# Optimization experiments

Measured on AMD Instinct MI355X. Metric: run time of the kernel, lower is better.

## Reference

```python
import jax, jax.numpy as jnp
import numpy as np

B, L, S, D, H, DH = 32, 96, 96, 512, 8, 64  # d_ff = S*S = 9216


def setup_inputs() -> dict:
    key = jax.random.key(0)
    ks = jax.random.split(key, 13)
    sc = 0.02
    inp = {
        "queries": jax.random.normal(ks[0], (B, L, D), jnp.float32),
        "keys": jax.random.normal(ks[1], (B, S, D), jnp.float32),
        "values": jax.random.normal(ks[2], (B, S, D), jnp.float32),
        "attn_mask": jnp.zeros((B, L, S), dtype=bool),
        # projections stored as (in, out); torch Linear is x @ W.T + b
        "Wq": jax.random.normal(ks[3], (D, H * DH), jnp.float32) * sc,
        "bq": jnp.zeros((H * DH,), jnp.float32),
        "Wk": jax.random.normal(ks[4], (D, H * DH), jnp.float32) * sc,
        "bk": jnp.zeros((H * DH,), jnp.float32),
        "Wv": jax.random.normal(ks[5], (D, H * DH), jnp.float32) * sc,
        "bv": jnp.zeros((H * DH,), jnp.float32),
        # core_value initialized as softmax over rank dim, as in the module
        "core": jax.nn.softmax(jax.random.normal(ks[6], (H, DH), jnp.float32), axis=-1),
        "Wo": jax.random.normal(ks[7], (S * S, D), jnp.float32) * sc,
        "bo": jnp.zeros((D,), jnp.float32),
    }
    return inp


def reference(queries, keys, values, attn_mask, Wq, bq, Wk, bk, Wv, bv, core, Wo, bo):
    b, l, _ = queries.shape
    s = keys.shape[1]
    h, d = core.shape
    # NOTE: the original uses .view(H, B, L, -1) on a (B, L, H*d) tensor —
    # a raw reshape, NOT a transpose. Replicate faithfully.
    q = (queries @ Wq + bq).reshape(h, b, l, d)
    k = (keys @ Wk + bk).reshape(h, b, s, d)
    v = (values @ Wv + bv).reshape(h, b, s, d)
    # per-head rank-d CP contraction, summed over heads, averaged by 1/H
    full = jnp.einsum("nh,nbih,nbjh,nbkh->bijk", core, q, k, v) / h  # [B,L,S,S]
    full = full.reshape(b, l, s * s)
    out = full @ Wo + bo  # [B, L, D]
    return out
```

## Files before the change

kernel.cpp:

```cpp
#include <hip/hip_runtime.h>
#include <hip/hip_bf16.h>
#include <stdint.h>

using bf16 = __hip_bfloat16;
typedef float v4f __attribute__((ext_vector_type(4)));
typedef short short8 __attribute__((ext_vector_type(8)));


__device__ __forceinline__ void async_cp16(void* l, const void* g) {
  __builtin_amdgcn_global_load_lds(
      (const __attribute__((address_space(1))) void*)(uintptr_t)g,
      (__attribute__((address_space(3))) void*)(uintptr_t)l, 16, 0, 0);
}

__global__ __launch_bounds__(256) void transpose_f32_bf16(
    const float* __restrict__ src, bf16* __restrict__ dst, int K, int N) {
  __shared__ bf16 T[32][33];
  const int k0 = blockIdx.x * 32, n0 = blockIdx.y * 32;
  const int t = threadIdx.x;
  const int r = t >> 3, c = (t & 7) * 4;
  float4 v = *reinterpret_cast<const float4*>(src + (size_t)(k0 + r) * N + n0 + c);
  T[c + 0][r] = __float2bfloat16(v.x);
  T[c + 1][r] = __float2bfloat16(v.y);
  T[c + 2][r] = __float2bfloat16(v.z);
  T[c + 3][r] = __float2bfloat16(v.w);
  __syncthreads();
  union { uint2 u; bf16 h[4]; } o;
  o.h[0] = T[r][c + 0]; o.h[1] = T[r][c + 1];
  o.h[2] = T[r][c + 2]; o.h[3] = T[r][c + 3];
  *reinterpret_cast<uint2*>(dst + (size_t)(n0 + r) * K + k0 + c) = o.u;
}

#define PJ_LD 72

__global__ __launch_bounds__(256) void proj_mfma(
    const float* __restrict__ X0, const float* __restrict__ X1,
    const float* __restrict__ X2,
    const bf16* __restrict__ WT0, const bf16* __restrict__ WT1,
    const bf16* __restrict__ WT2,
    const float* __restrict__ b0, const float* __restrict__ b1,
    const float* __restrict__ b2, const float* __restrict__ core,
    bf16* __restrict__ O0, bf16* __restrict__ O1, bf16* __restrict__ O2) {
  const int z = blockIdx.z;
  const float* X   = z == 0 ? X0  : (z == 1 ? X1  : X2);
  const bf16* WT   = z == 0 ? WT0 : (z == 1 ? WT1 : WT2);
  const float* bia = z == 0 ? b0  : (z == 1 ? b1  : b2);
  bf16* O          = z == 0 ? O0  : (z == 1 ? O1  : O2);

  __shared__ __align__(16) bf16 As[64 * PJ_LD];
  __shared__ __align__(16) bf16 Bs[64 * PJ_LD];
  const int t = threadIdx.x, w = t >> 6, lane = t & 63;
  const int wr = w >> 1, wc = w & 1, m16 = lane & 15, q = lane >> 4;
  const int bm = blockIdx.x * 64, bn = blockIdx.y * 64;

  v4f acc[2][2] = {};

  for (int k0 = 0; k0 < 512; k0 += 64) {
    __syncthreads();
    #pragma unroll
    for (int c = t; c < 1024; c += 256) {
      const int row = c >> 4, col = (c & 15) * 4;
      float4 v = *reinterpret_cast<const float4*>(
          X + (size_t)(bm + row) * 512 + k0 + col);
      union { uint2 u; bf16 h[4]; } o;
      o.h[0] = __float2bfloat16(v.x); o.h[1] = __float2bfloat16(v.y);
      o.h[2] = __float2bfloat16(v.z); o.h[3] = __float2bfloat16(v.w);
      *reinterpret_cast<uint2*>(&As[row * PJ_LD + col]) = o.u;
    }
    #pragma unroll
    for (int c = t; c < 512; c += 256) {
      const int row = c >> 3, col = (c & 7) * 8;
      *reinterpret_cast<uint4*>(&Bs[row * PJ_LD + col]) =
          *reinterpret_cast<const uint4*>(WT + (size_t)(bn + row) * 512 + k0 + col);
    }
    __syncthreads();

    #pragma unroll
    for (int s = 0; s < 2; s++) {
      const int koff = s * 32 + q * 8;
      short8 af[2], bfr[2];
      #pragma unroll
      for (int mt = 0; mt < 2; mt++)
        af[mt] = *reinterpret_cast<const short8*>(
            &As[(wr * 32 + mt * 16 + m16) * PJ_LD + koff]);
      #pragma unroll
      for (int nt = 0; nt < 2; nt++)
        bfr[nt] = *reinterpret_cast<const short8*>(
            &Bs[(wc * 32 + nt * 16 + m16) * PJ_LD + koff]);
      #pragma unroll
      for (int mt = 0; mt < 2; mt++)
        #pragma unroll
        for (int nt = 0; nt < 2; nt++)
          acc[mt][nt] = __builtin_amdgcn_mfma_f32_16x16x32_bf16(
              af[mt], bfr[nt], acc[mt][nt], 0, 0, 0);
    }
  }

  const bool isQ = (z == 0);
  const int nblk = bm / 384;
  #pragma unroll
  for (int mt = 0; mt < 2; mt++)
    #pragma unroll
    for (int nt = 0; nt < 2; nt++)
      #pragma unroll
      for (int r = 0; r < 4; r++) {
        const int row = bm + wr * 32 + mt * 16 + q * 4 + r;
        const int col = bn + wc * 32 + nt * 16 + m16;
        float v = acc[mt][nt][r] + bia[col];
        if (isQ) v *= core[nblk * 64 + (col & 63)] * 0.125f;
        O[(size_t)row * 512 + col] = __float2bfloat16(v);
      }
}

__global__ __launch_bounds__(256) void stage_b_mfma(
    const bf16* __restrict__ AQ, const bf16* __restrict__ KPb,
    const bf16* __restrict__ VPb, bf16* __restrict__ FULL) {
  const int b = blockIdx.y;
  const int i0 = blockIdx.x * 2;

  __shared__ __align__(16) bf16 smem[19456];
  bf16* Ks0 = smem;
  bf16* Ks1 = smem + 6144;
  bf16* Vs  = smem + 12288;
  bf16* aqs = smem + 18432;

  const int t = threadIdx.x;
  const int w = t >> 6, lane = t & 63;
  const int wr = w >> 1, wc = w & 1;
  const int m16 = lane & 15, q = lane >> 4;
  const int l8 = lane >> 3, l7 = lane & 7;

  if (t < 128) {
    const int isel = t & 1, n = t >> 4, seg = (t >> 1) & 7;
    *reinterpret_cast<uint4*>(&aqs[isel * 512 + n * 64 + seg * 8]) =
        *reinterpret_cast<const uint4*>(
            AQ + (size_t)n * 196608 + b * 6144 + (i0 + isel) * 64 + seg * 8);
  }

  union U8 { uint4 u; bf16 h[8]; };
  const int colq = (t & 7) * 8;
  const int rowk = t >> 3;
  const int krow7 = rowk & 7;

  U8 kk[3];
  {
    const bf16* Kp = KPb + b * 6144;
    #pragma unroll
    for (int c3 = 0; c3 < 3; c3++)
      kk[c3].u = *reinterpret_cast<const uint4*>(Kp + (t + c3 * 256) * 8);
  }

  v4f acc[2][3][3] = {};

  for (int n = 0; n < 8; n++) {
    __syncthreads();
    const bf16* Vp = VPb + (size_t)n * 196608 + b * 6144;
    #pragma unroll
    for (int c = 0; c < 3; c++) {
      const int r0 = (w * 3 + c) * 8;
      async_cp16(&Vs[(w * 3 + c) * 512],
                 Vp + (r0 + l8) * 64 + (l7 ^ l8) * 8);
    }
    float a0f[8], a1f[8];
    {
      U8 a0, a1;
      a0.u = *reinterpret_cast<const uint4*>(&aqs[n * 64 + colq]);
      a1.u = *reinterpret_cast<const uint4*>(&aqs[512 + n * 64 + colq]);
      #pragma unroll
      for (int e = 0; e < 8; e++) {
        a0f[e] = __bfloat162float(a0.h[e]);
        a1f[e] = __bfloat162float(a1.h[e]);
      }
    }
    #pragma unroll
    for (int c3 = 0; c3 < 3; c3++) {
      U8 s0, s1;
      #pragma unroll
      for (int e = 0; e < 8; e++) {
        const float kv = __bfloat162float(kk[c3].h[e]);
        s0.h[e] = __float2bfloat16(kv * a0f[e]);
        s1.h[e] = __float2bfloat16(kv * a1f[e]);
      }
      const int phys = (rowk + 32 * c3) * 64 + (l7 ^ krow7) * 8;
      *reinterpret_cast<uint4*>(&Ks0[phys]) = s0.u;
      *reinterpret_cast<uint4*>(&Ks1[phys]) = s1.u;
    }
    __syncthreads();
    if (n < 7) {
      const bf16* Kp1 = KPb + (size_t)(n + 1) * 196608 + b * 6144;
      #pragma unroll
      for (int c3 = 0; c3 < 3; c3++)
        kk[c3].u = *reinterpret_cast<const uint4*>(Kp1 + (t + c3 * 256) * 8);
    }

    #pragma unroll
    for (int s = 0; s < 2; s++) {
      const int pc = ((s * 4 + q) ^ (m16 & 7)) * 8;
      short8 bfr[3], af0[3], af1[3];
      #pragma unroll
      for (int cc = 0; cc < 3; cc++)
        bfr[cc] = *reinterpret_cast<const short8*>(
            &Vs[(wc * 48 + cc * 16 + m16) * 64 + pc]);
      #pragma unroll
      for (int a = 0; a < 3; a++) {
        af0[a] = *reinterpret_cast<const short8*>(
            &Ks0[(wr * 48 + a * 16 + m16) * 64 + pc]);
        af1[a] = *reinterpret_cast<const short8*>(
            &Ks1[(wr * 48 + a * 16 + m16) * 64 + pc]);
      }
      #pragma unroll
      for (int a = 0; a < 3; a++)
        #pragma unroll
        for (int cc = 0; cc < 3; cc++) {
          acc[0][a][cc] = __builtin_amdgcn_mfma_f32_16x16x32_bf16(
              af0[a], bfr[cc], acc[0][a][cc], 0, 0, 0);
          acc[1][a][cc] = __builtin_amdgcn_mfma_f32_16x16x32_bf16(
              af1[a], bfr[cc], acc[1][a][cc], 0, 0, 0);
        }
    }
  }

  __syncthreads();
  #pragma unroll
  for (int isel = 0; isel < 2; isel++)
    #pragma unroll
    for (int a = 0; a < 3; a++)
      #pragma unroll
      for (int cc = 0; cc < 3; cc++) {
        const int j0 = wr * 48 + a * 16, k0c = wc * 48 + cc * 16;
        #pragma unroll
        for (int r = 0; r < 4; r++)
          smem[isel * 9216 + (j0 + q * 4 + r) * 96 + k0c + m16] =
              __float2bfloat16(acc[isel][a][cc][r]);
      }
  __syncthreads();
  const size_t obase = (size_t)(b * 96 + i0) * 9216;
  #pragma unroll
  for (int c = t; c < 2304; c += 256)
    *reinterpret_cast<uint4*>(FULL + obase + c * 8) =
        *reinterpret_cast<const uint4*>(&smem[c * 8]);
}

__global__ __launch_bounds__(256) void init_out(
    const float* __restrict__ bo, float* __restrict__ out) {
  const int idx = (blockIdx.x * 256 + threadIdx.x) * 4;
  *reinterpret_cast<float4*>(out + idx) =
      *reinterpret_cast<const float4*>(bo + (idx & 511));
}

__global__ __launch_bounds__(256) void stage_c_mfma(
    const bf16* __restrict__ FULL, const bf16* __restrict__ WoT,
    float* __restrict__ out) {
  const int bm = blockIdx.x * 128, bn = blockIdx.y * 64;
  const int kbase = blockIdx.z * 2304;
  __shared__ __align__(16) bf16 As[128 * 128];
  __shared__ __align__(16) bf16 Bs[64 * 128];
  const int t = threadIdx.x;
  const int w = t >> 6, lane = t & 63;
  const int m16 = lane & 15, q = lane >> 4;
  const int l16 = lane >> 4, l15 = lane & 15;

  v4f acc[2][4] = {};

  for (int k0 = kbase; k0 < kbase + 2304; k0 += 128) {
    __syncthreads();
    #pragma unroll
    for (int c = 0; c < 8; c++) {
      const int row = (w * 8 + c) * 4 + l16;
      const int lch = l15 ^ (row & 7);
      async_cp16(&As[(w * 8 + c) * 512],
                 FULL + (size_t)(bm + row) * 9216 + k0 + lch * 8);
    }
    #pragma unroll
    for (int c = 0; c < 4; c++) {
      const int row = (w * 4 + c) * 4 + l16;
      const int lch = l15 ^ (row & 7);
      async_cp16(&Bs[(w * 4 + c) * 512],
                 WoT + (size_t)(bn + row) * 9216 + k0 + lch * 8);
    }
    __syncthreads();

    #pragma unroll
    for (int s = 0; s < 4; s++) {
      const int pc = ((s * 4 + q) ^ (m16 & 7)) * 8;
      short8 af[2], bfr[4];
      #pragma unroll
      for (int mt = 0; mt < 2; mt++)
        af[mt] = *reinterpret_cast<const short8*>(
            &As[(w * 32 + mt * 16 + m16) * 128 + pc]);
      #pragma unroll
      for (int nt = 0; nt < 4; nt++)
        bfr[nt] = *reinterpret_cast<const short8*>(
            &Bs[(nt * 16 + m16) * 128 + pc]);
      #pragma unroll
      for (int mt = 0; mt < 2; mt++)
        #pragma unroll
        for (int nt = 0; nt < 4; nt++)
          acc[mt][nt] = __builtin_amdgcn_mfma_f32_16x16x32_bf16(
              af[mt], bfr[nt], acc[mt][nt], 0, 0, 0);
    }
  }

  #pragma unroll
  for (int mt = 0; mt < 2; mt++)
    #pragma unroll
    for (int nt = 0; nt < 4; nt++)
      #pragma unroll
      for (int r = 0; r < 4; r++) {
        const int row = bm + w * 32 + mt * 16 + q * 4 + r;
        const int col = bn + nt * 16 + m16;
        atomicAdd(&out[(size_t)row * 512 + col], acc[mt][nt][r]);
      }
}

extern "C" void kernel_launch(void* const* d_in, const int* in_sizes, int n_in,
                              void* d_out, int out_size, void* d_ws, size_t ws_size,
                              hipStream_t stream) {
  const float* queries = (const float*)d_in[0];
  const float* keys    = (const float*)d_in[1];
  const float* values  = (const float*)d_in[2];
  const float* Wq   = (const float*)d_in[4];
  const float* bq   = (const float*)d_in[5];
  const float* Wk   = (const float*)d_in[6];
  const float* bk   = (const float*)d_in[7];
  const float* Wv   = (const float*)d_in[8];
  const float* bv   = (const float*)d_in[9];
  const float* core = (const float*)d_in[10];
  const float* Wo   = (const float*)d_in[11];
  const float* bo   = (const float*)d_in[12];
  float* out = (float*)d_out;

  char* ws = (char*)d_ws;
  bf16* AQb = (bf16*)(ws);
  bf16* KPb = (bf16*)(ws + 3145728);
  bf16* VPb = (bf16*)(ws + 6291456);
  bf16* WTq = (bf16*)(ws + 9437184);
  bf16* WTk = (bf16*)(ws + 9961472);
  bf16* WTv = (bf16*)(ws + 10485760);
  bf16* WoT = (bf16*)(ws + 11010048);
  bf16* FULL = (bf16*)(ws + 20447232);

  const dim3 blk(256);

  transpose_f32_bf16<<<dim3(16, 16),  blk, 0, stream>>>(Wq, WTq, 512, 512);
  transpose_f32_bf16<<<dim3(16, 16),  blk, 0, stream>>>(Wk, WTk, 512, 512);
  transpose_f32_bf16<<<dim3(16, 16),  blk, 0, stream>>>(Wv, WTv, 512, 512);
  transpose_f32_bf16<<<dim3(288, 16), blk, 0, stream>>>(Wo, WoT, 9216, 512);

  proj_mfma<<<dim3(48, 8, 3), blk, 0, stream>>>(
      queries, keys, values, WTq, WTk, WTv, bq, bk, bv, core, AQb, KPb, VPb);

  stage_b_mfma<<<dim3(48, 32), blk, 0, stream>>>(AQb, KPb, VPb, FULL);

  init_out<<<dim3(1536), blk, 0, stream>>>(bo, out);
  stage_c_mfma<<<dim3(24, 8, 4), blk, 0, stream>>>(FULL, WoT, out);
}
```

Baseline: 224.0 us.

## Load MFMA operands directly from global, drop LDS staging, merge transposes

Merges the four weight-transpose launches into one kernel. proj_mfma now reads MFMA operand fragments straight from global memory with no LDS tiles or barriers, with each wave covering 32x64 and the block covering 128 rows. stage_b does the same: it loads K, V and AQ fragments directly from global and forms the scaled K in registers. This removes LDS traffic and __syncthreads stalls, but relies on L1/L2 to absorb redundant, poorly coalesced global reads, and K/V rows are now reloaded by several waves.

Result: slower. 277.3 us (+23.8%).

```diff
diff --git a/kernel.cpp b/kernel.cpp
--- a/kernel.cpp
+++ b/kernel.cpp
@@ -5,6 +5,7 @@
 using bf16 = __hip_bfloat16;
 typedef float v4f __attribute__((ext_vector_type(4)));
 typedef short short8 __attribute__((ext_vector_type(8)));
+union U8 { uint4 u; bf16 h[8]; short8 s; };
 
 
 __device__ __forceinline__ void async_cp16(void* l, const void* g) {
@@ -13,10 +14,23 @@
       (__attribute__((address_space(3))) void*)(uintptr_t)l, 16, 0, 0);
 }
 
-__global__ __launch_bounds__(256) void transpose_f32_bf16(
-    const float* __restrict__ src, bf16* __restrict__ dst, int K, int N) {
+__global__ __launch_bounds__(256) void transpose_all(
+    const float* __restrict__ Wo, const float* __restrict__ Wq,
+    const float* __restrict__ Wk, const float* __restrict__ Wv,
+    bf16* __restrict__ WoT, bf16* __restrict__ WTq,
+    bf16* __restrict__ WTk, bf16* __restrict__ WTv) {
   __shared__ bf16 T[32][33];
-  const int k0 = blockIdx.x * 32, n0 = blockIdx.y * 32;
+  const int bid = blockIdx.x;
+  const float* src; bf16* dst; int K, N, kx, ny;
+  if (bid < 4608) {
+    src = Wo; dst = WoT; K = 9216; N = 512; kx = bid % 288; ny = bid / 288;
+  } else {
+    const int r = bid - 4608, which = r >> 8, rr = r & 255;
+    kx = rr & 15; ny = rr >> 4; K = 512; N = 512;
+    src = which == 0 ? Wq : (which == 1 ? Wk : Wv);
+    dst = which == 0 ? WTq : (which == 1 ? WTk : WTv);
+  }
+  const int k0 = kx * 32, n0 = ny * 32;
   const int t = threadIdx.x;
   const int r = t >> 3, c = (t & 7) * 4;
   float4 v = *reinterpret_cast<const float4*>(src + (size_t)(k0 + r) * N + n0 + c);
@@ -31,8 +45,6 @@
   *reinterpret_cast<uint2*>(dst + (size_t)(n0 + r) * K + k0 + c) = o.u;
 }
 
-#define PJ_LD 72
-
 __global__ __launch_bounds__(256) void proj_mfma(
     const float* __restrict__ X0, const float* __restrict__ X1,
     const float* __restrict__ X2,
@@ -42,55 +54,43 @@
     const float* __restrict__ b2, const float* __restrict__ core,
     bf16* __restrict__ O0, bf16* __restrict__ O1, bf16* __restrict__ O2) {
   const int z = blockIdx.z;
-  const float* X   = z == 0 ? X0  : (z == 1 ? X1  : X2);
+  const float* X   = z == 0 ? X0 : (z == 1 ? X1 : X2);
   const bf16* WT   = z == 0 ? WT0 : (z == 1 ? WT1 : WT2);
-  const float* bia = z == 0 ? b0  : (z == 1 ? b1  : b2);
-  bf16* O          = z == 0 ? O0  : (z == 1 ? O1  : O2);
-
-  __shared__ __align__(16) bf16 As[64 * PJ_LD];
-  __shared__ __align__(16) bf16 Bs[64 * PJ_LD];
+  const float* bia = z == 0 ? b0 : (z == 1 ? b1 : b2);
+  bf16* O          = z == 0 ? O0 : (z == 1 ? O1 : O2);
+
   const int t = threadIdx.x, w = t >> 6, lane = t & 63;
-  const int wr = w >> 1, wc = w & 1, m16 = lane & 15, q = lane >> 4;
-  const int bm = blockIdx.x * 64, bn = blockIdx.y * 64;
-
-  v4f acc[2][2] = {};
-
+  const int m16 = lane & 15, q = lane >> 4;
+  const int bm = blockIdx.x * 128, bn = blockIdx.y * 64;
+
+  v4f acc[2][4] = {};
+
+  #pragma unroll
   for (int k0 = 0; k0 < 512; k0 += 64) {
-    __syncthreads();
-    #pragma unroll
-    for (int c = t; c < 1024; c += 256) {
-      const int row = c >> 4, col = (c & 15) * 4;
-      float4 v = *reinterpret_cast<const float4*>(
-          X + (size_t)(bm + row) * 512 + k0 + col);
-      union { uint2 u; bf16 h[4]; } o;
-      o.h[0] = __float2bfloat16(v.x); o.h[1] = __float2bfloat16(v.y);
-      o.h[2] = __float2bfloat16(v.z); o.h[3] = __float2bfloat16(v.w);
-      *reinterpret_cast<uint2*>(&As[row * PJ_LD + col]) = o.u;
-    }
-    #pragma unroll
-    for (int c = t; c < 512; c += 256) {
-      const int row = c >> 3, col = (c & 7) * 8;
-      *reinterpret_cast<uint4*>(&Bs[row * PJ_LD + col]) =
-          *reinterpret_cast<const uint4*>(WT + (size_t)(bn + row) * 512 + k0 + col);
-    }
-    __syncthreads();
-
     #pragma unroll
     for (int s = 0; s < 2; s++) {
-      const int koff = s * 32 + q * 8;
-      short8 af[2], bfr[2];
+      const int kof = k0 + s * 32 + q * 8;
+      short8 af[2], bfr[4];
+      #pragma unroll
+      for (int mt = 0; mt < 2; mt++) {
+        const float* xp = X + (size_t)(bm + w * 32 + mt * 16 + m16) * 512 + kof;
+        float4 x0 = reinterpret_cast<const float4*>(xp)[0];
+        float4 x1 = reinterpret_cast<const float4*>(xp)[1];
+        U8 a;
+        a.h[0] = __float2bfloat16(x0.x); a.h[1] = __float2bfloat16(x0.y);
+        a.h[2] = __float2bfloat16(x0.z); a.h[3] = __float2bfloat16(x0.w);
+        a.h[4] = __float2bfloat16(x1.x); a.h[5] = __float2bfloat16(x1.y);
+        a.h[6] = __float2bfloat16(x1.z); a.h[7] = __float2bfloat16(x1.w);
+        af[mt] = a.s;
+      }
+      #pragma unroll
+      for (int nt = 0; nt < 4; nt++)
+        bfr[nt] = *reinterpret_cast<const short8*>(
+            WT + (size_t)(bn + nt * 16 + m16) * 512 + kof);
       #pragma unroll
       for (int mt = 0; mt < 2; mt++)
-        af[mt] = *reinterpret_cast<const short8*>(
-            &As[(wr * 32 + mt * 16 + m16) * PJ_LD + koff]);
-      #pragma unroll
-      for (int nt = 0; nt < 2; nt++)
-        bfr[nt] = *reinterpret_cast<const short8*>(
-            &Bs[(wc * 32 + nt * 16 + m16) * PJ_LD + koff]);
-      #pragma unroll
-      for (int mt = 0; mt < 2; mt++)
-        #pragma unroll
-        for (int nt = 0; nt < 2; nt++)
+        #pragma unroll
+        for (int nt = 0; nt < 4; nt++)
           acc[mt][nt] = __builtin_amdgcn_mfma_f32_16x16x32_bf16(
               af[mt], bfr[nt], acc[mt][nt], 0, 0, 0);
     }
@@ -101,11 +101,11 @@
   #pragma unroll
   for (int mt = 0; mt < 2; mt++)
     #pragma unroll
-    for (int nt = 0; nt < 2; nt++)
+    for (int nt = 0; nt < 4; nt++)
       #pragma unroll
       for (int r = 0; r < 4; r++) {
-        const int row = bm + wr * 32 + mt * 16 + q * 4 + r;
-        const int col = bn + wc * 32 + nt * 16 + m16;
+        const int row = bm + w * 32 + mt * 16 + q * 4 + r;
+        const int col = bn + nt * 16 + m16;
         float v = acc[mt][nt][r] + bia[col];
         if (isQ) v *= core[nblk * 64 + (col & 63)] * 0.125f;
         O[(size_t)row * 512 + col] = __float2bfloat16(v);
@@ -118,95 +118,50 @@
   const int b = blockIdx.y;
   const int i0 = blockIdx.x * 2;
 
-  __shared__ __align__(16) bf16 smem[19456];
-  bf16* Ks0 = smem;
-  bf16* Ks1 = smem + 6144;
-  bf16* Vs  = smem + 12288;
-  bf16* aqs = smem + 18432;
+  __shared__ __align__(16) bf16 smem[2 * 9216];
 
   const int t = threadIdx.x;
   const int w = t >> 6, lane = t & 63;
   const int wr = w >> 1, wc = w & 1;
   const int m16 = lane & 15, q = lane >> 4;
-  const int l8 = lane >> 3, l7 = lane & 7;
-
-  if (t < 128) {
-    const int isel = t & 1, n = t >> 4, seg = (t >> 1) & 7;
-    *reinterpret_cast<uint4*>(&aqs[isel * 512 + n * 64 + seg * 8]) =
-        *reinterpret_cast<const uint4*>(
-            AQ + (size_t)n * 196608 + b * 6144 + (i0 + isel) * 64 + seg * 8);
-  }
-
-  union U8 { uint4 u; bf16 h[8]; };
-  const int colq = (t & 7) * 8;
-  const int rowk = t >> 3;
-  const int krow7 = rowk & 7;
-
-  U8 kk[3];
-  {
-    const bf16* Kp = KPb + b * 6144;
-    #pragma unroll
-    for (int c3 = 0; c3 < 3; c3++)
-      kk[c3].u = *reinterpret_cast<const uint4*>(Kp + (t + c3 * 256) * 8);
-  }
-
+
+  const size_t slab = (size_t)b * 6144;
   v4f acc[2][3][3] = {};
 
   for (int n = 0; n < 8; n++) {
-    __syncthreads();
-    const bf16* Vp = VPb + (size_t)n * 196608 + b * 6144;
-    #pragma unroll
-    for (int c = 0; c < 3; c++) {
-      const int r0 = (w * 3 + c) * 8;
-      async_cp16(&Vs[(w * 3 + c) * 512],
-                 Vp + (r0 + l8) * 64 + (l7 ^ l8) * 8);
-    }
-    float a0f[8], a1f[8];
-    {
+    const bf16* Kp = KPb + (size_t)n * 196608 + slab;
+    const bf16* Vp = VPb + (size_t)n * 196608 + slab;
+    const bf16* Ap = AQ + (size_t)n * 196608 + slab + i0 * 64;
+    #pragma unroll
+    for (int s = 0; s < 2; s++) {
+      const int kof = s * 32 + q * 8;
       U8 a0, a1;
-      a0.u = *reinterpret_cast<const uint4*>(&aqs[n * 64 + colq]);
-      a1.u = *reinterpret_cast<const uint4*>(&aqs[512 + n * 64 + colq]);
+      a0.u = *reinterpret_cast<const uint4*>(Ap + kof);
+      a1.u = *reinterpret_cast<const uint4*>(Ap + 64 + kof);
+      float a0f[8], a1f[8];
       #pragma unroll
       for (int e = 0; e < 8; e++) {
         a0f[e] = __bfloat162float(a0.h[e]);
         a1f[e] = __bfloat162float(a1.h[e]);
       }
-    }
-    #pragma unroll
-    for (int c3 = 0; c3 < 3; c3++) {
-      U8 s0, s1;
-      #pragma unroll
-      for (int e = 0; e < 8; e++) {
-        const float kv = __bfloat162float(kk[c3].h[e]);
-        s0.h[e] = __float2bfloat16(kv * a0f[e]);
-        s1.h[e] = __float2bfloat16(kv * a1f[e]);
-      }
-      const int phys = (rowk + 32 * c3) * 64 + (l7 ^ krow7) * 8;
-      *reinterpret_cast<uint4*>(&Ks0[phys]) = s0.u;
-      *reinterpret_cast<uint4*>(&Ks1[phys]) = s1.u;
-    }
-    __syncthreads();
-    if (n < 7) {
-      const bf16* Kp1 = KPb + (size_t)(n + 1) * 196608 + b * 6144;
-      #pragma unroll
-      for (int c3 = 0; c3 < 3; c3++)
-        kk[c3].u = *reinterpret_cast<const uint4*>(Kp1 + (t + c3 * 256) * 8);
-    }
-
-    #pragma unroll
-    for (int s = 0; s < 2; s++) {
-      const int pc = ((s * 4 + q) ^ (m16 & 7)) * 8;
       short8 bfr[3], af0[3], af1[3];
       #pragma unroll
       for (int cc = 0; cc < 3; cc++)
         bfr[cc] = *reinterpret_cast<const short8*>(
-            &Vs[(wc * 48 + cc * 16 + m16) * 64 + pc]);
+            Vp + (wc * 48 + cc * 16 + m16) * 64 + kof);
       #pragma unroll
       for (int a = 0; a < 3; a++) {
-        af0[a] = *reinterpret_cast<const short8*>(
-            &Ks0[(wr * 48 + a * 16 + m16) * 64 + pc]);
-        af1[a] = *reinterpret_cast<const short8*>(
-            &Ks1[(wr * 48 + a * 16 + m16) * 64 + pc]);
+        U8 kv, s0, s1;
+        kv.u = *reinterpret_cast<const uint4*>(
+            Kp + (wr * 48 + a * 16 + m16) * 64 + kof);
+        #pragma unroll
+        for (int e = 0; e < 8; e++) {
+          const float kf = __bfloat162float(kv.h[e]);
+          s0.h[e] = __float2bfloat16(kf * a0f[e]);
+          s1.h[e] = __float2bfloat16(kf * a1f[e]);
+        }
+        af0[a] = s0.s;
+        af1[a] = s1.s;
       }
       #pragma unroll
       for (int a = 0; a < 3; a++)
@@ -220,7 +175,6 @@
     }
   }
 
-  __syncthreads();
   #pragma unroll
   for (int isel = 0; isel < 2; isel++)
     #pragma unroll
@@ -342,12 +296,10 @@
 
   const dim3 blk(256);
 
-  transpose_f32_bf16<<<dim3(16, 16),  blk, 0, stream>>>(Wq, WTq, 512, 512);
-  transpose_f32_bf16<<<dim3(16, 16),  blk, 0, stream>>>(Wk, WTk, 512, 512);
-  transpose_f32_bf16<<<dim3(16, 16),  blk, 0, stream>>>(Wv, WTv, 512, 512);
-  transpose_f32_bf16<<<dim3(288, 16), blk, 0, stream>>>(Wo, WoT, 9216, 512);
-
-  proj_mfma<<<dim3(48, 8, 3), blk, 0, stream>>>(
+  transpose_all<<<dim3(5376), blk, 0, stream>>>(
+      Wo, Wq, Wk, Wv, WoT, WTq, WTk, WTv);
+
+  proj_mfma<<<dim3(24, 8, 3), blk, 0, stream>>>(
       queries, keys, values, WTq, WTk, WTv, bq, bk, bv, core, AQb, KPb, VPb);
 
   stage_b_mfma<<<dim3(48, 32), blk, 0, stream>>>(AQb, KPb, VPb, FULL);
```

## Fuse prep kernels and retile projection GEMM with async LDS loads

Applied to the files above, without the earlier changes.

Merges the four weight transposes, the bias init of the output, and a new fp32-to-bf16 conversion of the activation inputs into a single prep launch. The projection GEMM now reads the pre-converted bf16 inputs through async global-to-LDS copies with an XOR-swizzled layout, and uses 128x64 tiles with a K-step of 128, reusing the stage_c tiling scheme. The bf16 input copies live in the FULL buffer region, which stage_b overwrites later. This cuts launch count and conversion work inside the GEMM, at the cost of an extra global round-trip for the activations.

Result: faster. 205.4 us (-8.3%).

```diff
diff --git a/kernel.cpp b/kernel.cpp
--- a/kernel.cpp
+++ b/kernel.cpp
@@ -13,84 +13,126 @@
       (__attribute__((address_space(3))) void*)(uintptr_t)l, 16, 0, 0);
 }
 
-__global__ __launch_bounds__(256) void transpose_f32_bf16(
-    const float* __restrict__ src, bf16* __restrict__ dst, int K, int N) {
-  __shared__ bf16 T[32][33];
-  const int k0 = blockIdx.x * 32, n0 = blockIdx.y * 32;
-  const int t = threadIdx.x;
-  const int r = t >> 3, c = (t & 7) * 4;
-  float4 v = *reinterpret_cast<const float4*>(src + (size_t)(k0 + r) * N + n0 + c);
-  T[c + 0][r] = __float2bfloat16(v.x);
-  T[c + 1][r] = __float2bfloat16(v.y);
-  T[c + 2][r] = __float2bfloat16(v.z);
-  T[c + 3][r] = __float2bfloat16(v.w);
-  __syncthreads();
-  union { uint2 u; bf16 h[4]; } o;
-  o.h[0] = T[r][c + 0]; o.h[1] = T[r][c + 1];
-  o.h[2] = T[r][c + 2]; o.h[3] = T[r][c + 3];
-  *reinterpret_cast<uint2*>(dst + (size_t)(n0 + r) * K + k0 + c) = o.u;
-}
-
-#define PJ_LD 72
+__global__ __launch_bounds__(256) void prep(
+    const float* __restrict__ Wo, const float* __restrict__ Wq,
+    const float* __restrict__ Wk, const float* __restrict__ Wv,
+    const float* __restrict__ Xq, const float* __restrict__ Xk,
+    const float* __restrict__ Xv, const float* __restrict__ bo,
+    bf16* __restrict__ WoT, bf16* __restrict__ WTq,
+    bf16* __restrict__ WTk, bf16* __restrict__ WTv,
+    bf16* __restrict__ Xbq, bf16* __restrict__ Xbk, bf16* __restrict__ Xbv,
+    float* __restrict__ out) {
+  const int bid = blockIdx.x, t = threadIdx.x;
+  if (bid < 5376) {
+    __shared__ bf16 T[32][33];
+    const float* src; bf16* dst; int K, N, kx, ny;
+    if (bid < 4608) {
+      src = Wo; dst = WoT; K = 9216; N = 512; kx = bid % 288; ny = bid / 288;
+    } else {
+      const int r = bid - 4608, which = r >> 8, rr = r & 255;
+      kx = rr & 15; ny = rr >> 4; K = 512; N = 512;
+      src = which == 0 ? Wq : (which == 1 ? Wk : Wv);
+      dst = which == 0 ? WTq : (which == 1 ? WTk : WTv);
+    }
+    const int k0 = kx * 32, n0 = ny * 32;
+    const int r = t >> 3, c = (t & 7) * 4;
+    float4 v = *reinterpret_cast<const float4*>(src + (size_t)(k0 + r) * N + n0 + c);
+    T[c + 0][r] = __float2bfloat16(v.x);
+    T[c + 1][r] = __float2bfloat16(v.y);
+    T[c + 2][r] = __float2bfloat16(v.z);
+    T[c + 3][r] = __float2bfloat16(v.w);
+    __syncthreads();
+    union { uint2 u; bf16 h[4]; } o;
+    o.h[0] = T[r][c + 0]; o.h[1] = T[r][c + 1];
+    o.h[2] = T[r][c + 2]; o.h[3] = T[r][c + 3];
+    *reinterpret_cast<uint2*>(dst + (size_t)(n0 + r) * K + k0 + c) = o.u;
+  } else if (bid < 6528) {
+    const int r = bid - 5376;
+    const int which = r / 384, blk = r % 384;
+    const float* src = which == 0 ? Xq : (which == 1 ? Xk : Xv);
+    bf16* dst = which == 0 ? Xbq : (which == 1 ? Xbk : Xbv);
+    const int base = blk * 4096 + t * 16;
+    float4 a = *reinterpret_cast<const float4*>(src + base);
+    float4 b = *reinterpret_cast<const float4*>(src + base + 4);
+    float4 c = *reinterpret_cast<const float4*>(src + base + 8);
+    float4 d = *reinterpret_cast<const float4*>(src + base + 12);
+    union { uint4 u; bf16 h[8]; } o1, o2;
+    o1.h[0] = __float2bfloat16(a.x); o1.h[1] = __float2bfloat16(a.y);
+    o1.h[2] = __float2bfloat16(a.z); o1.h[3] = __float2bfloat16(a.w);
+    o1.h[4] = __float2bfloat16(b.x); o1.h[5] = __float2bfloat16(b.y);
+    o1.h[6] = __float2bfloat16(b.z); o1.h[7] = __float2bfloat16(b.w);
+    o2.h[0] = __float2bfloat16(c.x); o2.h[1] = __float2bfloat16(c.y);
+    o2.h[2] = __float2bfloat16(c.z); o2.h[3] = __float2bfloat16(c.w);
+    o2.h[4] = __float2bfloat16(d.x); o2.h[5] = __float2bfloat16(d.y);
+    o2.h[6] = __float2bfloat16(d.z); o2.h[7] = __float2bfloat16(d.w);
+    *reinterpret_cast<uint4*>(dst + base) = o1.u;
+    *reinterpret_cast<uint4*>(dst + base + 8) = o2.u;
+  } else {
+    const int r = bid - 6528;
+    const int idx = (r * 256 + t) * 4;
+    *reinterpret_cast<float4*>(out + idx) =
+        *reinterpret_cast<const float4*>(bo + (idx & 511));
+  }
+}
 
 __global__ __launch_bounds__(256) void proj_mfma(
-    const float* __restrict__ X0, const float* __restrict__ X1,
-    const float* __restrict__ X2,
+    const bf16* __restrict__ Xb0, const bf16* __restrict__ Xb1,
+    const bf16* __restrict__ Xb2,
     const bf16* __restrict__ WT0, const bf16* __restrict__ WT1,
     const bf16* __restrict__ WT2,
     const float* __restrict__ b0, const float* __restrict__ b1,
     const float* __restrict__ b2, const float* __restrict__ core,
     bf16* __restrict__ O0, bf16* __restrict__ O1, bf16* __restrict__ O2) {
   const int z = blockIdx.z;
-  const float* X   = z == 0 ? X0  : (z == 1 ? X1  : X2);
+  const bf16* X    = z == 0 ? Xb0 : (z == 1 ? Xb1 : Xb2);
   const bf16* WT   = z == 0 ? WT0 : (z == 1 ? WT1 : WT2);
-  const float* bia = z == 0 ? b0  : (z == 1 ? b1  : b2);
-  bf16* O          = z == 0 ? O0  : (z == 1 ? O1  : O2);
-
-  __shared__ __align__(16) bf16 As[64 * PJ_LD];
-  __shared__ __align__(16) bf16 Bs[64 * PJ_LD];
-  const int t = threadIdx.x, w = t >> 6, lane = t & 63;
-  const int wr = w >> 1, wc = w & 1, m16 = lane & 15, q = lane >> 4;
-  const int bm = blockIdx.x * 64, bn = blockIdx.y * 64;
-
-  v4f acc[2][2] = {};
-
-  for (int k0 = 0; k0 < 512; k0 += 64) {
-    __syncthreads();
-    #pragma unroll
-    for (int c = t; c < 1024; c += 256) {
-      const int row = c >> 4, col = (c & 15) * 4;
-      float4 v = *reinterpret_cast<const float4*>(
-          X + (size_t)(bm + row) * 512 + k0 + col);
-      union { uint2 u; bf16 h[4]; } o;
-      o.h[0] = __float2bfloat16(v.x); o.h[1] = __float2bfloat16(v.y);
-      o.h[2] = __float2bfloat16(v.z); o.h[3] = __float2bfloat16(v.w);
-      *reinterpret_cast<uint2*>(&As[row * PJ_LD + col]) = o.u;
-    }
-    #pragma unroll
-    for (int c = t; c < 512; c += 256) {
-      const int row = c >> 3, col = (c & 7) * 8;
-      *reinterpret_cast<uint4*>(&Bs[row * PJ_LD + col]) =
-          *reinterpret_cast<const uint4*>(WT + (size_t)(bn + row) * 512 + k0 + col);
-    }
-    __syncthreads();
-
-    #pragma unroll
-    for (int s = 0; s < 2; s++) {
-      const int koff = s * 32 + q * 8;
-      short8 af[2], bfr[2];
+  const float* bia = z == 0 ? b0 : (z == 1 ? b1 : b2);
+  bf16* O          = z == 0 ? O0 : (z == 1 ? O1 : O2);
+
+  const int bm = blockIdx.x * 128, bn = blockIdx.y * 64;
+  __shared__ __align__(16) bf16 As[128 * 128];
+  __shared__ __align__(16) bf16 Bs[64 * 128];
+  const int t = threadIdx.x;
+  const int w = t >> 6, lane = t & 63;
+  const int m16 = lane & 15, q = lane >> 4;
+  const int l16 = lane >> 4, l15 = lane & 15;
+
+  v4f acc[2][4] = {};
+
+  for (int k0 = 0; k0 < 512; k0 += 128) {
+    __syncthreads();
+    #pragma unroll
+    for (int c = 0; c < 8; c++) {
+      const int row = (w * 8 + c) * 4 + l16;
+      const int lch = l15 ^ (row & 7);
+      async_cp16(&As[(w * 8 + c) * 512],
+                 X + (size_t)(bm + row) * 512 + k0 + lch * 8);
+    }
+    #pragma unroll
+    for (int c = 0; c < 4; c++) {
+      const int row = (w * 4 + c) * 4 + l16;
+      const int lch = l15 ^ (row & 7);
+      async_cp16(&Bs[(w * 4 + c) * 512],
+                 WT + (size_t)(bn + row) * 512 + k0 + lch * 8);
+    }
+    __syncthreads();
+
+    #pragma unroll
+    for (int s = 0; s < 4; s++) {
+      const int pc = ((s * 4 + q) ^ (m16 & 7)) * 8;
+      short8 af[2], bfr[4];
       #pragma unroll
       for (int mt = 0; mt < 2; mt++)
         af[mt] = *reinterpret_cast<const short8*>(
-            &As[(wr * 32 + mt * 16 + m16) * PJ_LD + koff]);
-      #pragma unroll
-      for (int nt = 0; nt < 2; nt++)
+            &As[(w * 32 + mt * 16 + m16) * 128 + pc]);
+      #pragma unroll
+      for (int nt = 0; nt < 4; nt++)
         bfr[nt] = *reinterpret_cast<const short8*>(
-            &Bs[(wc * 32 + nt * 16 + m16) * PJ_LD + koff]);
+            &Bs[(nt * 16 + m16) * 128 + pc]);
       #pragma unroll
       for (int mt = 0; mt < 2; mt++)
         #pragma unroll
-        for (int nt = 0; nt < 2; nt++)
+        for (int nt = 0; nt < 4; nt++)
           acc[mt][nt] = __builtin_amdgcn_mfma_f32_16x16x32_bf16(
               af[mt], bfr[nt], acc[mt][nt], 0, 0, 0);
     }
@@ -101,11 +143,11 @@
   #pragma unroll
   for (int mt = 0; mt < 2; mt++)
     #pragma unroll
-    for (int nt = 0; nt < 2; nt++)
+    for (int nt = 0; nt < 4; nt++)
       #pragma unroll
       for (int r = 0; r < 4; r++) {
-        const int row = bm + wr * 32 + mt * 16 + q * 4 + r;
-        const int col = bn + wc * 32 + nt * 16 + m16;
+        const int row = bm + w * 32 + mt * 16 + q * 4 + r;
+        const int col = bn + nt * 16 + m16;
         float v = acc[mt][nt][r] + bia[col];
         if (isQ) v *= core[nblk * 64 + (col & 63)] * 0.125f;
         O[(size_t)row * 512 + col] = __float2bfloat16(v);
@@ -239,13 +281,6 @@
   for (int c = t; c < 2304; c += 256)
     *reinterpret_cast<uint4*>(FULL + obase + c * 8) =
         *reinterpret_cast<const uint4*>(&smem[c * 8]);
-}
-
-__global__ __launch_bounds__(256) void init_out(
-    const float* __restrict__ bo, float* __restrict__ out) {
-  const int idx = (blockIdx.x * 256 + threadIdx.x) * 4;
-  *reinterpret_cast<float4*>(out + idx) =
-      *reinterpret_cast<const float4*>(bo + (idx & 511));
 }
 
 __global__ __launch_bounds__(256) void stage_c_mfma(
@@ -339,19 +374,20 @@
   bf16* WTv = (bf16*)(ws + 10485760);
   bf16* WoT = (bf16*)(ws + 11010048);
   bf16* FULL = (bf16*)(ws + 20447232);
+  bf16* Xbq = FULL;
+  bf16* Xbk = FULL + 1572864;
+  bf16* Xbv = FULL + 3145728;
 
   const dim3 blk(256);
 
-  transpose_f32_bf16<<<dim3(16, 16),  blk, 0, stream>>>(Wq, WTq, 512, 512);
-  transpose_f32_bf16<<<dim3(16, 16),  blk, 0, stream>>>(Wk, WTk, 512, 512);
-  transpose_f32_bf16<<<dim3(16, 16),  blk, 0, stream>>>(Wv, WTv, 512, 512);
-  transpose_f32_bf16<<<dim3(288, 16), blk, 0, stream>>>(Wo, WoT, 9216, 512);
-
-  proj_mfma<<<dim3(48, 8, 3), blk, 0, stream>>>(
-      queries, keys, values, WTq, WTk, WTv, bq, bk, bv, core, AQb, KPb, VPb);
+  prep<<<dim3(8064), blk, 0, stream>>>(
+      Wo, Wq, Wk, Wv, queries, keys, values, bo,
+      WoT, WTq, WTk, WTv, Xbq, Xbk, Xbv, out);
+
+  proj_mfma<<<dim3(24, 8, 3), blk, 0, stream>>>(
+      Xbq, Xbk, Xbv, WTq, WTk, WTv, bq, bk, bv, core, AQb, KPb, VPb);
 
   stage_b_mfma<<<dim3(48, 32), blk, 0, stream>>>(AQb, KPb, VPb, FULL);
 
-  init_out<<<dim3(1536), blk, 0, stream>>>(bo, out);
   stage_c_mfma<<<dim3(24, 8, 4), blk, 0, stream>>>(FULL, WoT, out);
 }
```
